# Kernel optimization log

Measured on AMD Instinct MI355X. Metric: run time of the kernel, lower is better.

Reference implementation:

```python
import jax, jax.numpy as jnp
import numpy as np

B, N, H = 8, 256, 768
P = 128          # path_hidden_size
HEADS = 12
D = H // HEADS   # 64
EPS = 1e-5


def layer_norm(x, g, b):
    mu = jnp.mean(x, axis=-1, keepdims=True)
    var = jnp.mean((x - mu) ** 2, axis=-1, keepdims=True)
    return (x - mu) * jax.lax.rsqrt(var + EPS) * g + b


def setup_inputs() -> dict:
    key = jax.random.key(0)
    ks = jax.random.split(key, 16)
    s = 0.02
    return {
        "nodes": jax.random.normal(ks[0], (B, N, H), jnp.float32),
        "bias": jax.random.normal(ks[1], (B, HEADS, N, N), jnp.float32),
        "paths": jax.random.normal(ks[2], (B, N, N, P), jnp.float32),
        "Wq": jax.random.normal(ks[3], (H, H), jnp.float32) * s,
        "bq": jnp.zeros((H,), jnp.float32),
        "Wk": jax.random.normal(ks[4], (H, H), jnp.float32) * s,
        "bk": jnp.zeros((H,), jnp.float32),
        "Wv": jax.random.normal(ks[5], (H, H), jnp.float32) * s,
        "bv": jnp.zeros((H,), jnp.float32),
        "Wsk": jax.random.normal(ks[6], (P, D), jnp.float32) * s,
        "bsk": jnp.zeros((D,), jnp.float32),
        "Wsv": jax.random.normal(ks[7], (P, D), jnp.float32) * s,
        "bsv": jnp.zeros((D,), jnp.float32),
        "Wo": jax.random.normal(ks[8], (H, H), jnp.float32) * s,
        "bo": jnp.zeros((H,), jnp.float32),
        "g_path": jnp.ones((P,), jnp.float32),
        "b_path": jnp.zeros((P,), jnp.float32),
        "g_out": jnp.ones((H,), jnp.float32),
        "b_out": jnp.zeros((H,), jnp.float32),
    }


def reference(nodes, bias, paths, Wq, bq, Wk, bk, Wv, bv, Wsk, bsk, Wsv, bsv,
              Wo, bo, g_path, b_path, g_out, b_out):
    # q/k/v: [B,N,H] -> [B,heads,N,D]
    def split(x):
        return x.reshape(B, N, HEADS, D).transpose(0, 2, 1, 3)

    q = split(nodes @ Wq + bq)
    k = split(nodes @ Wk + bk)
    v = split(nodes @ Wv + bv)

    pn = layer_norm(paths, g_path, b_path)          # [B,N,N,P]
    struct_k = pn @ Wsk + bsk                       # [B,N,N,D]
    struct_v = pn @ Wsv + bsv                       # [B,N,N,D]

    q = q * (D ** -0.5)
    # content scores + per-query-row structural scores + bias
    w = (jnp.einsum('bhqd,bhkd->bhqk', q, k)
         + jnp.einsum('bhqd,bqkd->bhqk', q, struct_k)
         + bias)
    w = jax.nn.softmax(w, axis=-1)                  # [B,heads,N,N]

    out = (jnp.einsum('bhqk,bhkd->bhqd', w, v)
           + jnp.einsum('bhqk,bqkd->bhqd', w, struct_v))
    out = out.transpose(0, 2, 1, 3).reshape(B, N, H)  # combine heads
    out = jax.nn.relu(out @ Wo + bo)
    # dropout is identity in eval mode
    return layer_norm(nodes + out, g_out, b_out)
```

## Files before the change

kernel.cpp:

```cpp
#include <hip/hip_runtime.h>
#include <stdint.h>

#define Bb 8
#define Nn 256
#define Hh 768
#define Pp 128
#define HEADS 12
#define Dd 64
#define EPSf 1e-5f

typedef __attribute__((ext_vector_type(8))) short bhalf8;
typedef __attribute__((ext_vector_type(4))) float f32x4;

__device__ __forceinline__ unsigned short f2bf(float f) {
    union { float f; unsigned u; } v; v.f = f;
    unsigned r = v.u + 0x7FFFu + ((v.u >> 16) & 1u);
    return (unsigned short)(r >> 16);
}
__device__ __forceinline__ float bflo(unsigned u) {
    union { unsigned u; float f; } v; v.u = u << 16; return v.f;
}
__device__ __forceinline__ float bfhi(unsigned u) {
    union { unsigned u; float f; } v; v.u = u & 0xFFFF0000u; return v.f;
}

__global__ __launch_bounds__(256) void k_transpose_bf16(const float* __restrict__ in,
                                                        unsigned short* __restrict__ out,
                                                        int R, int C) {
    __shared__ float tile[32][33];
    int c0 = blockIdx.x * 32, r0 = blockIdx.y * 32;
    int tx = threadIdx.x & 31, ty = threadIdx.x >> 5;
    for (int i = ty; i < 32; i += 8) {
        int r = r0 + i, c = c0 + tx;
        tile[i][tx] = (r < R && c < C) ? in[(size_t)r * C + c] : 0.f;
    }
    __syncthreads();
    for (int i = ty; i < 32; i += 8) {
        int c = c0 + i, r = r0 + tx;
        if (c < C && r < R) out[(size_t)c * R + r] = f2bf(tile[tx][i]);
    }
}

__global__ __launch_bounds__(256) void k_qkv(const float* __restrict__ nodes,
                                             const unsigned short* __restrict__ Wt,
                                             const float* __restrict__ bq, const float* __restrict__ bk,
                                             const float* __restrict__ bv,
                                             float* __restrict__ qs, float* __restrict__ kk,
                                             float* __restrict__ vv) {
    __shared__ __align__(16) unsigned short Alds[64 * 72];
    __shared__ __align__(16) unsigned short Blds[128 * 72];
    int tid = threadIdx.x;
    int m0 = blockIdx.y * 64;
    int n0 = blockIdx.x * 128;
    int w = tid >> 6, lane = tid & 63;
    int wm = w >> 1, wn = w & 1;
    int lm = lane & 15, lq = lane >> 4;
    f32x4 acc[2][4];
#pragma unroll
    for (int i = 0; i < 2; i++)
#pragma unroll
        for (int j = 0; j < 4; j++) acc[i][j] = (f32x4){0.f, 0.f, 0.f, 0.f};

    for (int kt = 0; kt < 768; kt += 64) {
#pragma unroll
        for (int t = 0; t < 4; t++) {
            int c = t * 256 + tid;
            int row = c >> 4, cc = c & 15;
            float4 v = *(const float4*)(nodes + (size_t)(m0 + row) * 768 + kt + cc * 4);
            unsigned u0 = (unsigned)f2bf(v.x) | ((unsigned)f2bf(v.y) << 16);
            unsigned u1 = (unsigned)f2bf(v.z) | ((unsigned)f2bf(v.w) << 16);
            uint2 uu; uu.x = u0; uu.y = u1;
            *(uint2*)(Alds + row * 72 + cc * 4) = uu;
        }
#pragma unroll
        for (int t = 0; t < 4; t++) {
            int c = t * 256 + tid;
            int n = c >> 3, kc = c & 7;
            uint4 v = *(const uint4*)(Wt + (size_t)(n0 + n) * 768 + kt + kc * 8);
            *(uint4*)(Blds + n * 72 + kc * 8) = v;
        }
        __syncthreads();
#pragma unroll
        for (int ks = 0; ks < 2; ks++) {
            bhalf8 af[2];
#pragma unroll
            for (int mi = 0; mi < 2; mi++)
                af[mi] = *(const bhalf8*)(Alds + (wm * 32 + mi * 16 + lm) * 72 + ks * 32 + lq * 8);
#pragma unroll
            for (int nt = 0; nt < 4; nt++) {
                bhalf8 bf = *(const bhalf8*)(Blds + (wn * 64 + nt * 16 + lm) * 72 + ks * 32 + lq * 8);
#pragma unroll
                for (int mi = 0; mi < 2; mi++)
                    acc[mi][nt] = __builtin_amdgcn_mfma_f32_16x16x32_bf16(af[mi], bf, acc[mi][nt], 0, 0, 0);
            }
        }
        __syncthreads();
    }
    int wsel = n0 / 768;
    int nb = n0 % 768;
    const float* bias = (wsel == 0) ? bq : (wsel == 1) ? bk : bv;
    float* dst = (wsel == 0) ? qs : (wsel == 1) ? kk : vv;
    float scale = (wsel == 0) ? 0.125f : 1.0f;
#pragma unroll
    for (int mi = 0; mi < 2; mi++)
#pragma unroll
        for (int nt = 0; nt < 4; nt++)
#pragma unroll
            for (int r = 0; r < 4; r++) {
                int row = m0 + wm * 32 + mi * 16 + lq * 4 + r;
                int col = nb + wn * 64 + nt * 16 + lm;
                int hh = col >> 6, d = col & 63;
                int b = row >> 8, qn = row & 255;
                float val = (acc[mi][nt][r] + bias[col]) * scale;
                dst[(((size_t)b * HEADS + hh) * Nn + qn) * Dd + d] = val;
            }
}

__global__ __launch_bounds__(256) void k_scores(const float* __restrict__ qs,
                                                const float* __restrict__ kk,
                                                const float* __restrict__ bias,
                                                float* __restrict__ wg) {
    __shared__ __align__(16) unsigned short Alds[64 * 72];
    __shared__ __align__(16) unsigned short Blds[64 * 72];
    int tid = threadIdx.x;
    int bh = blockIdx.z;
    int m0 = blockIdx.y * 64;
    int n0 = blockIdx.x * 64;
    int w = tid >> 6, lane = tid & 63, lm = lane & 15, lq = lane >> 4;
    const float* Abase = qs + ((size_t)bh * Nn + m0) * Dd;
    const float* Bbase = kk + ((size_t)bh * Nn + n0) * Dd;
#pragma unroll
    for (int t = 0; t < 4; t++) {
        int c = t * 256 + tid;
        int row = c >> 4, cc = c & 15;
        float4 va = *(const float4*)(Abase + (size_t)row * 64 + cc * 4);
        uint2 ua;
        ua.x = (unsigned)f2bf(va.x) | ((unsigned)f2bf(va.y) << 16);
        ua.y = (unsigned)f2bf(va.z) | ((unsigned)f2bf(va.w) << 16);
        *(uint2*)(Alds + row * 72 + cc * 4) = ua;
        float4 vb = *(const float4*)(Bbase + (size_t)row * 64 + cc * 4);
        uint2 ub;
        ub.x = (unsigned)f2bf(vb.x) | ((unsigned)f2bf(vb.y) << 16);
        ub.y = (unsigned)f2bf(vb.z) | ((unsigned)f2bf(vb.w) << 16);
        *(uint2*)(Blds + row * 72 + cc * 4) = ub;
    }
    __syncthreads();
    f32x4 acc[4];
#pragma unroll
    for (int i = 0; i < 4; i++) acc[i] = (f32x4){0.f, 0.f, 0.f, 0.f};
#pragma unroll
    for (int ks = 0; ks < 2; ks++) {
        bhalf8 af = *(const bhalf8*)(Alds + (w * 16 + lm) * 72 + ks * 32 + lq * 8);
#pragma unroll
        for (int nt = 0; nt < 4; nt++) {
            bhalf8 bf = *(const bhalf8*)(Blds + (nt * 16 + lm) * 72 + ks * 32 + lq * 8);
            acc[nt] = __builtin_amdgcn_mfma_f32_16x16x32_bf16(af, bf, acc[nt], 0, 0, 0);
        }
    }
#pragma unroll
    for (int nt = 0; nt < 4; nt++)
#pragma unroll
        for (int r = 0; r < 4; r++) {
            int row = m0 + w * 16 + lq * 4 + r;
            int col = n0 + nt * 16 + lm;
            size_t idx = ((size_t)bh * Nn + row) * Nn + col;
            wg[idx] = acc[nt][r] + bias[idx];
        }
}

__global__ __launch_bounds__(256) void k_structproj(const float* __restrict__ paths,
                                                    const unsigned short* __restrict__ Wskvt,
                                                    const float* __restrict__ gp, const float* __restrict__ bp,
                                                    const float* __restrict__ bsk, const float* __restrict__ bsv,
                                                    unsigned short* __restrict__ skv) {
    __shared__ __align__(16) unsigned short pn[64 * 136];
    __shared__ __align__(16) unsigned short Bt[128 * 136];
    int tid = threadIdx.x;
    size_t r0 = (size_t)blockIdx.x * 64;
    int w = tid >> 6, lane = tid & 63, lm = lane & 15, lq = lane >> 4;
#pragma unroll
    for (int t = 0; t < 8; t++) {
        int c = t * 256 + tid;
        int n = c >> 4, kc = c & 15;
        uint4 v = *(const uint4*)(Wskvt + n * 128 + kc * 8);
        *(uint4*)(Bt + n * 136 + kc * 8) = v;
    }
    float2 g2 = *(const float2*)(gp + lane * 2);
    float2 b2 = *(const float2*)(bp + lane * 2);
    float2 xr[16];
#pragma unroll
    for (int i = 0; i < 16; i++) {
        size_t row = r0 + w * 16 + i;
        xr[i] = *(const float2*)(paths + row * 128 + lane * 2);
    }
#pragma unroll
    for (int i = 0; i < 16; i++) {
        float2 x = xr[i];
        float s = x.x + x.y, s2 = x.x * x.x + x.y * x.y;
#pragma unroll
        for (int mk = 32; mk; mk >>= 1) {
            s += __shfl_xor(s, mk);
            s2 += __shfl_xor(s2, mk);
        }
        float mu = s * (1.f / 128.f);
        float var = s2 * (1.f / 128.f) - mu * mu;
        float rs = rsqrtf(var + EPSf);
        float p0 = (x.x - mu) * rs * g2.x + b2.x;
        float p1 = (x.y - mu) * rs * g2.y + b2.y;
        unsigned u = (unsigned)f2bf(p0) | ((unsigned)f2bf(p1) << 16);
        *(unsigned*)(pn + (w * 16 + i) * 136 + lane * 2) = u;
    }
    __syncthreads();
    f32x4 acc[8];
#pragma unroll
    for (int i = 0; i < 8; i++) acc[i] = (f32x4){0.f, 0.f, 0.f, 0.f};
#pragma unroll
    for (int ks = 0; ks < 4; ks++) {
        bhalf8 af = *(const bhalf8*)(pn + (w * 16 + lm) * 136 + ks * 32 + lq * 8);
#pragma unroll
        for (int nt = 0; nt < 8; nt++) {
            bhalf8 bf = *(const bhalf8*)(Bt + (nt * 16 + lm) * 136 + ks * 32 + lq * 8);
            acc[nt] = __builtin_amdgcn_mfma_f32_16x16x32_bf16(af, bf, acc[nt], 0, 0, 0);
        }
    }
#pragma unroll
    for (int nt = 0; nt < 8; nt++) {
        int col = nt * 16 + lm;
        float bias = (col < 64) ? bsk[col] : bsv[col - 64];
#pragma unroll
        for (int r = 0; r < 4; r++) {
            size_t grow = r0 + w * 16 + lq * 4 + r;
            skv[grow * 128 + col] = f2bf(acc[nt][r] + bias);
        }
    }
}

__global__ __launch_bounds__(256) void k_attn(const float* __restrict__ qs,
                                              const unsigned short* __restrict__ skv,
                                              float* __restrict__ wg,
                                              float* __restrict__ attn) {
    __shared__ __align__(16) unsigned skl[256 * 36];
    __shared__ __align__(16) float qv[12 * 64];
    __shared__ __align__(16) float wl[12 * 260];
    __shared__ float redm[4], reds[4];
    int tid = threadIdx.x;
    int bq = blockIdx.x;
    int b = bq >> 8, q = bq & 255;
    int lane = tid & 63, wid = tid >> 6;
#pragma unroll
    for (int i = 0; i < 3; i++) {
        int idx = i * 256 + tid;
        int h = idx >> 6, d = idx & 63;
        qv[idx] = qs[(((size_t)b * HEADS + h) * Nn + q) * Dd + d];
    }
    const unsigned short* rowb = skv + (size_t)bq * 256 * 128;
#pragma unroll
    for (int i = 0; i < 8; i++) {
        int c = i * 256 + tid;
        int k = c >> 3, j = c & 7;
        uint4 v = *(const uint4*)(rowb + (size_t)k * 128 + j * 8);
        *(uint4*)(skl + k * 36 + j * 4) = v;
    }
    __syncthreads();
    for (int h = 0; h < 12; h++) {
        float s = 0.f;
#pragma unroll
        for (int j = 0; j < 32; j++) {
            unsigned u = skl[tid * 36 + j];
            float2 q2 = *(const float2*)(qv + h * 64 + 2 * j);
            s += q2.x * bflo(u) + q2.y * bfhi(u);
        }
        size_t widx = (((size_t)b * HEADS + h) * Nn + q) * Nn;
        s += wg[widx + tid];
        float m = s;
#pragma unroll
        for (int mk = 32; mk; mk >>= 1) m = fmaxf(m, __shfl_xor(m, mk));
        if (lane == 0) redm[wid] = m;
        __syncthreads();
        m = fmaxf(fmaxf(redm[0], redm[1]), fmaxf(redm[2], redm[3]));
        float p = __expf(s - m);
        float ps = p;
#pragma unroll
        for (int mk = 32; mk; mk >>= 1) ps += __shfl_xor(ps, mk);
        if (lane == 0) reds[wid] = ps;
        __syncthreads();
        float sum = reds[0] + reds[1] + reds[2] + reds[3];
        float pr = p / sum;
        wl[h * 260 + tid] = pr;
        wg[widx + tid] = pr;
        __syncthreads();
    }
#pragma unroll
    for (int i = 0; i < 8; i++) {
        int c = i * 256 + tid;
        int k = c >> 3, j = c & 7;
        uint4 v = *(const uint4*)(rowb + (size_t)k * 128 + 64 + j * 8);
        *(uint4*)(skl + k * 36 + j * 4) = v;
    }
    __syncthreads();
#pragma unroll
    for (int i = 0; i < 3; i++) {
        int idx = i * 256 + tid;
        int h = idx >> 6, d = idx & 63;
        int jw = d >> 1;
        float o = 0.f;
        if (d & 1) {
            for (int k = 0; k < 256; k += 4) {
                float4 w4 = *(const float4*)(wl + h * 260 + k);
                o += w4.x * bfhi(skl[(k + 0) * 36 + jw]);
                o += w4.y * bfhi(skl[(k + 1) * 36 + jw]);
                o += w4.z * bfhi(skl[(k + 2) * 36 + jw]);
                o += w4.w * bfhi(skl[(k + 3) * 36 + jw]);
            }
        } else {
            for (int k = 0; k < 256; k += 4) {
                float4 w4 = *(const float4*)(wl + h * 260 + k);
                o += w4.x * bflo(skl[(k + 0) * 36 + jw]);
                o += w4.y * bflo(skl[(k + 1) * 36 + jw]);
                o += w4.z * bflo(skl[(k + 2) * 36 + jw]);
                o += w4.w * bflo(skl[(k + 3) * 36 + jw]);
            }
        }
        attn[(size_t)bq * Hh + idx] = o;
    }
}

__global__ __launch_bounds__(256) void k_ctxout(const float* __restrict__ wg,
                                                const float* __restrict__ vv,
                                                float* __restrict__ attn) {
    __shared__ __align__(16) float Al[64 * 68];
    __shared__ __align__(16) float Bl[64 * 68];
    int tid = threadIdx.x;
    int bh = blockIdx.y;
    int m0 = blockIdx.x * 64;
    int b = bh / 12, h = bh % 12;
    int tx = tid & 15, ty = tid >> 4;
    int c0 = tx * 4, r0 = ty * 4;
    float acc[4][4];
#pragma unroll
    for (int i = 0; i < 4; i++)
#pragma unroll
        for (int j = 0; j < 4; j++) acc[i][j] = 0.f;
    const float* Abase = wg + ((size_t)bh * Nn + m0) * Nn;
    const float* Bbase = vv + (size_t)bh * Nn * Dd;
    for (int kt = 0; kt < 256; kt += 64) {
#pragma unroll
        for (int t = 0; t < 4; t++) {
            int c = t * 256 + tid;
            int row = c >> 4, cc = c & 15;
            *(float4*)(Al + row * 68 + cc * 4) = *(const float4*)(Abase + (size_t)row * 256 + kt + cc * 4);
            *(float4*)(Bl + row * 68 + cc * 4) = *(const float4*)(Bbase + (size_t)(kt + row) * 64 + cc * 4);
        }
        __syncthreads();
#pragma unroll 8
        for (int k = 0; k < 64; k++) {
            float4 bv4 = *(const float4*)(Bl + k * 68 + c0);
            float a0 = Al[(r0 + 0) * 68 + k];
            float a1 = Al[(r0 + 1) * 68 + k];
            float a2 = Al[(r0 + 2) * 68 + k];
            float a3 = Al[(r0 + 3) * 68 + k];
            acc[0][0] += a0 * bv4.x; acc[0][1] += a0 * bv4.y; acc[0][2] += a0 * bv4.z; acc[0][3] += a0 * bv4.w;
            acc[1][0] += a1 * bv4.x; acc[1][1] += a1 * bv4.y; acc[1][2] += a1 * bv4.z; acc[1][3] += a1 * bv4.w;
            acc[2][0] += a2 * bv4.x; acc[2][1] += a2 * bv4.y; acc[2][2] += a2 * bv4.z; acc[2][3] += a2 * bv4.w;
            acc[3][0] += a3 * bv4.x; acc[3][1] += a3 * bv4.y; acc[3][2] += a3 * bv4.z; acc[3][3] += a3 * bv4.w;
        }
        __syncthreads();
    }
#pragma unroll
    for (int i = 0; i < 4; i++)
#pragma unroll
        for (int j = 0; j < 4; j++) {
            size_t o = ((size_t)b * Nn + m0 + r0 + i) * Hh + h * 64 + c0 + j;
            attn[o] += acc[i][j];
        }
}

__global__ __launch_bounds__(256) void k_outproj(const float* __restrict__ attn,
                                                 const unsigned short* __restrict__ Wot,
                                                 const float* __restrict__ bo,
                                                 const float* __restrict__ nodes,
                                                 float* __restrict__ tmp) {
    __shared__ __align__(16) unsigned short Alds[64 * 72];
    __shared__ __align__(16) unsigned short Blds[128 * 72];
    int tid = threadIdx.x;
    int m0 = blockIdx.y * 64;
    int n0 = blockIdx.x * 128;
    int w = tid >> 6, lane = tid & 63;
    int wm = w >> 1, wn = w & 1;
    int lm = lane & 15, lq = lane >> 4;
    f32x4 acc[2][4];
#pragma unroll
    for (int i = 0; i < 2; i++)
#pragma unroll
        for (int j = 0; j < 4; j++) acc[i][j] = (f32x4){0.f, 0.f, 0.f, 0.f};
    for (int kt = 0; kt < 768; kt += 64) {
#pragma unroll
        for (int t = 0; t < 4; t++) {
            int c = t * 256 + tid;
            int row = c >> 4, cc = c & 15;
            float4 v = *(const float4*)(attn + (size_t)(m0 + row) * 768 + kt + cc * 4);
            uint2 uu;
            uu.x = (unsigned)f2bf(v.x) | ((unsigned)f2bf(v.y) << 16);
            uu.y = (unsigned)f2bf(v.z) | ((unsigned)f2bf(v.w) << 16);
            *(uint2*)(Alds + row * 72 + cc * 4) = uu;
        }
#pragma unroll
        for (int t = 0; t < 4; t++) {
            int c = t * 256 + tid;
            int n = c >> 3, kc = c & 7;
            uint4 v = *(const uint4*)(Wot + (size_t)(n0 + n) * 768 + kt + kc * 8);
            *(uint4*)(Blds + n * 72 + kc * 8) = v;
        }
        __syncthreads();
#pragma unroll
        for (int ks = 0; ks < 2; ks++) {
            bhalf8 af[2];
#pragma unroll
            for (int mi = 0; mi < 2; mi++)
                af[mi] = *(const bhalf8*)(Alds + (wm * 32 + mi * 16 + lm) * 72 + ks * 32 + lq * 8);
#pragma unroll
            for (int nt = 0; nt < 4; nt++) {
                bhalf8 bf = *(const bhalf8*)(Blds + (wn * 64 + nt * 16 + lm) * 72 + ks * 32 + lq * 8);
#pragma unroll
                for (int mi = 0; mi < 2; mi++)
                    acc[mi][nt] = __builtin_amdgcn_mfma_f32_16x16x32_bf16(af[mi], bf, acc[mi][nt], 0, 0, 0);
            }
        }
        __syncthreads();
    }
#pragma unroll
    for (int mi = 0; mi < 2; mi++)
#pragma unroll
        for (int nt = 0; nt < 4; nt++)
#pragma unroll
            for (int r = 0; r < 4; r++) {
                int row = m0 + wm * 32 + mi * 16 + lq * 4 + r;
                int col = n0 + wn * 64 + nt * 16 + lm;
                float val = acc[mi][nt][r] + bo[col];
                val = fmaxf(val, 0.f) + nodes[(size_t)row * 768 + col];
                tmp[(size_t)row * 768 + col] = val;
            }
}

__global__ __launch_bounds__(256) void k_finalln(const float* __restrict__ tmp,
                                                 const float* __restrict__ go,
                                                 const float* __restrict__ bout,
                                                 float* __restrict__ out) {
    __shared__ float rs1[4], rs2[4];
    int m = blockIdx.x, tid = threadIdx.x;
    int lane = tid & 63, wid = tid >> 6;
    const float* row = tmp + (size_t)m * 768;
    float x0 = row[tid], x1 = row[tid + 256], x2 = row[tid + 512];
    float s = x0 + x1 + x2;
    float s2 = x0 * x0 + x1 * x1 + x2 * x2;
#pragma unroll
    for (int mk = 32; mk; mk >>= 1) {
        s += __shfl_xor(s, mk);
        s2 += __shfl_xor(s2, mk);
    }
    if (lane == 0) { rs1[wid] = s; rs2[wid] = s2; }
    __syncthreads();
    s = rs1[0] + rs1[1] + rs1[2] + rs1[3];
    s2 = rs2[0] + rs2[1] + rs2[2] + rs2[3];
    float mu = s * (1.f / 768.f);
    float var = s2 * (1.f / 768.f) - mu * mu;
    float rstd = rsqrtf(var + EPSf);
    float* orow = out + (size_t)m * 768;
    orow[tid] = (x0 - mu) * rstd * go[tid] + bout[tid];
    orow[tid + 256] = (x1 - mu) * rstd * go[tid + 256] + bout[tid + 256];
    orow[tid + 512] = (x2 - mu) * rstd * go[tid + 512] + bout[tid + 512];
}

extern "C" void kernel_launch(void* const* d_in, const int* in_sizes, int n_in,
                              void* d_out, int out_size, void* d_ws, size_t ws_size,
                              hipStream_t stream) {
    const float* nodes = (const float*)d_in[0];
    const float* bias  = (const float*)d_in[1];
    const float* paths = (const float*)d_in[2];
    const float* Wq = (const float*)d_in[3];  const float* bq  = (const float*)d_in[4];
    const float* Wk = (const float*)d_in[5];  const float* bk  = (const float*)d_in[6];
    const float* Wv = (const float*)d_in[7];  const float* bv  = (const float*)d_in[8];
    const float* Wsk = (const float*)d_in[9]; const float* bsk = (const float*)d_in[10];
    const float* Wsv = (const float*)d_in[11];const float* bsv = (const float*)d_in[12];
    const float* Wo = (const float*)d_in[13]; const float* bo  = (const float*)d_in[14];
    const float* gp = (const float*)d_in[15]; const float* bp  = (const float*)d_in[16];
    const float* go = (const float*)d_in[17]; const float* bout= (const float*)d_in[18];
    float* out = (float*)d_out;

    char* ws = (char*)d_ws;
    size_t off = 0;
    auto carve = [&](size_t bytes) -> char* {
        char* p = ws + off;
        off += (bytes + 255) & ~(size_t)255;
        return p;
    };
    float* qs   = (float*)carve((size_t)Bb * HEADS * Nn * Dd * 4);
    float* kk   = (float*)carve((size_t)Bb * HEADS * Nn * Dd * 4);
    float* vv   = (float*)carve((size_t)Bb * HEADS * Nn * Dd * 4);
    float* wg   = (float*)carve((size_t)Bb * HEADS * Nn * Nn * 4);
    float* attn = (float*)carve((size_t)Bb * Nn * Hh * 4);
    float* tmp  = (float*)carve((size_t)Bb * Nn * Hh * 4);
    unsigned short* Wqkvt = (unsigned short*)carve((size_t)3 * 768 * 768 * 2);
    unsigned short* Wot   = (unsigned short*)carve((size_t)768 * 768 * 2);
    unsigned short* Wskvt = (unsigned short*)carve((size_t)128 * 128 * 2);
    unsigned short* skv   = (unsigned short*)carve((size_t)Bb * Nn * Nn * 128 * 2);
    (void)ws_size; (void)in_sizes; (void)n_in; (void)out_size;

    hipLaunchKernelGGL(k_transpose_bf16, dim3(24, 24), dim3(256), 0, stream, Wq, Wqkvt, 768, 768);
    hipLaunchKernelGGL(k_transpose_bf16, dim3(24, 24), dim3(256), 0, stream, Wk, Wqkvt + (size_t)768 * 768, 768, 768);
    hipLaunchKernelGGL(k_transpose_bf16, dim3(24, 24), dim3(256), 0, stream, Wv, Wqkvt + (size_t)2 * 768 * 768, 768, 768);
    hipLaunchKernelGGL(k_transpose_bf16, dim3(24, 24), dim3(256), 0, stream, Wo, Wot, 768, 768);
    hipLaunchKernelGGL(k_transpose_bf16, dim3(2, 4), dim3(256), 0, stream, Wsk, Wskvt, 128, 64);
    hipLaunchKernelGGL(k_transpose_bf16, dim3(2, 4), dim3(256), 0, stream, Wsv, Wskvt + (size_t)64 * 128, 128, 64);

    hipLaunchKernelGGL(k_qkv, dim3(18, 32), dim3(256), 0, stream, nodes, Wqkvt, bq, bk, bv, qs, kk, vv);
    hipLaunchKernelGGL(k_scores, dim3(4, 4, 96), dim3(256), 0, stream, qs, kk, bias, wg);
    hipLaunchKernelGGL(k_structproj, dim3(8192), dim3(256), 0, stream, paths, Wskvt, gp, bp, bsk, bsv, skv);
    hipLaunchKernelGGL(k_attn, dim3(2048), dim3(256), 0, stream, qs, skv, wg, attn);
    hipLaunchKernelGGL(k_ctxout, dim3(4, 96), dim3(256), 0, stream, wg, vv, attn);
    hipLaunchKernelGGL(k_outproj, dim3(6, 32), dim3(256), 0, stream, attn, Wot, bo, nodes, tmp);
    hipLaunchKernelGGL(k_finalln, dim3(2048), dim3(256), 0, stream, tmp, go, bout, out);
}
```

Baseline: 671.6 us.

## Use MFMA for per-query structural attention and coalesce structproj stores

The per-query attention kernel now computes the structural scores (q·struct_k) and the weighted sum over struct_v with bf16 MFMA instructions. It pads the 12 heads to 16 rows, replacing the scalar FMA loops that ran a barrier-heavy softmax once per head. The structural projection kernel loads paths with float4 and a 16-lane reduction, then stages its output through LDS so the bf16 writes to skv are coalesced 16-byte stores. The weight transposes are merged into two launches. The risks are wasted MFMA rows from the padding, bf16 rounding of q and the softmax probabilities, and strided scalar LDS gathers when building the B operand.

After: 557.4 us. 1.2x faster.

```diff
diff --git a/kernel.cpp b/kernel.cpp
--- a/kernel.cpp
+++ b/kernel.cpp
@@ -17,28 +17,39 @@
     unsigned r = v.u + 0x7FFFu + ((v.u >> 16) & 1u);
     return (unsigned short)(r >> 16);
 }
-__device__ __forceinline__ float bflo(unsigned u) {
-    union { unsigned u; float f; } v; v.u = u << 16; return v.f;
-}
-__device__ __forceinline__ float bfhi(unsigned u) {
-    union { unsigned u; float f; } v; v.u = u & 0xFFFF0000u; return v.f;
-}
-
-__global__ __launch_bounds__(256) void k_transpose_bf16(const float* __restrict__ in,
-                                                        unsigned short* __restrict__ out,
-                                                        int R, int C) {
+
+__global__ __launch_bounds__(256) void k_transpose4(const float* __restrict__ a0, const float* __restrict__ a1,
+                                                    const float* __restrict__ a2, const float* __restrict__ a3,
+                                                    unsigned short* __restrict__ o0, unsigned short* __restrict__ o1,
+                                                    unsigned short* __restrict__ o2, unsigned short* __restrict__ o3) {
     __shared__ float tile[32][33];
+    int z = blockIdx.z;
+    const float* in = (z == 0) ? a0 : (z == 1) ? a1 : (z == 2) ? a2 : a3;
+    unsigned short* out = (z == 0) ? o0 : (z == 1) ? o1 : (z == 2) ? o2 : o3;
+    const int R = 768, C = 768;
     int c0 = blockIdx.x * 32, r0 = blockIdx.y * 32;
     int tx = threadIdx.x & 31, ty = threadIdx.x >> 5;
-    for (int i = ty; i < 32; i += 8) {
-        int r = r0 + i, c = c0 + tx;
-        tile[i][tx] = (r < R && c < C) ? in[(size_t)r * C + c] : 0.f;
-    }
-    __syncthreads();
-    for (int i = ty; i < 32; i += 8) {
-        int c = c0 + i, r = r0 + tx;
-        if (c < C && r < R) out[(size_t)c * R + r] = f2bf(tile[tx][i]);
-    }
+    for (int i = ty; i < 32; i += 8)
+        tile[i][tx] = in[(size_t)(r0 + i) * C + c0 + tx];
+    __syncthreads();
+    for (int i = ty; i < 32; i += 8)
+        out[(size_t)(c0 + i) * R + r0 + tx] = f2bf(tile[tx][i]);
+}
+
+__global__ __launch_bounds__(256) void k_transpose_small(const float* __restrict__ a0, const float* __restrict__ a1,
+                                                         unsigned short* __restrict__ o0, unsigned short* __restrict__ o1) {
+    __shared__ float tile[32][33];
+    int z = blockIdx.z;
+    const float* in = (z == 0) ? a0 : a1;
+    unsigned short* out = (z == 0) ? o0 : o1;
+    const int R = 128, C = 64;
+    int c0 = blockIdx.x * 32, r0 = blockIdx.y * 32;
+    int tx = threadIdx.x & 31, ty = threadIdx.x >> 5;
+    for (int i = ty; i < 32; i += 8)
+        tile[i][tx] = in[(size_t)(r0 + i) * C + c0 + tx];
+    __syncthreads();
+    for (int i = ty; i < 32; i += 8)
+        out[(size_t)(c0 + i) * R + r0 + tx] = f2bf(tile[tx][i]);
 }
 
 __global__ __launch_bounds__(256) void k_qkv(const float* __restrict__ nodes,
@@ -67,9 +78,9 @@
             int c = t * 256 + tid;
             int row = c >> 4, cc = c & 15;
             float4 v = *(const float4*)(nodes + (size_t)(m0 + row) * 768 + kt + cc * 4);
-            unsigned u0 = (unsigned)f2bf(v.x) | ((unsigned)f2bf(v.y) << 16);
-            unsigned u1 = (unsigned)f2bf(v.z) | ((unsigned)f2bf(v.w) << 16);
-            uint2 uu; uu.x = u0; uu.y = u1;
+            uint2 uu;
+            uu.x = (unsigned)f2bf(v.x) | ((unsigned)f2bf(v.y) << 16);
+            uu.y = (unsigned)f2bf(v.z) | ((unsigned)f2bf(v.w) << 16);
             *(uint2*)(Alds + row * 72 + cc * 4) = uu;
         }
 #pragma unroll
@@ -185,30 +196,43 @@
         uint4 v = *(const uint4*)(Wskvt + n * 128 + kc * 8);
         *(uint4*)(Bt + n * 136 + kc * 8) = v;
     }
-    float2 g2 = *(const float2*)(gp + lane * 2);
-    float2 b2 = *(const float2*)(bp + lane * 2);
-    float2 xr[16];
-#pragma unroll
-    for (int i = 0; i < 16; i++) {
-        size_t row = r0 + w * 16 + i;
-        xr[i] = *(const float2*)(paths + row * 128 + lane * 2);
-    }
-#pragma unroll
-    for (int i = 0; i < 16; i++) {
-        float2 x = xr[i];
-        float s = x.x + x.y, s2 = x.x * x.x + x.y * x.y;
-#pragma unroll
-        for (int mk = 32; mk; mk >>= 1) {
+    float4 g0 = *(const float4*)(gp + lm * 4);
+    float4 g1 = *(const float4*)(gp + 64 + lm * 4);
+    float4 bb0 = *(const float4*)(bp + lm * 4);
+    float4 bb1 = *(const float4*)(bp + 64 + lm * 4);
+#pragma unroll
+    for (int it = 0; it < 4; it++) {
+        int row_l = w * 16 + it * 4 + lq;
+        size_t row = r0 + row_l;
+        const float* pr = paths + row * 128;
+        float4 x0 = *(const float4*)(pr + lm * 4);
+        float4 x1 = *(const float4*)(pr + 64 + lm * 4);
+        float s = (x0.x + x0.y) + (x0.z + x0.w) + (x1.x + x1.y) + (x1.z + x1.w);
+        float s2 = x0.x * x0.x + x0.y * x0.y + x0.z * x0.z + x0.w * x0.w
+                 + x1.x * x1.x + x1.y * x1.y + x1.z * x1.z + x1.w * x1.w;
+#pragma unroll
+        for (int mk = 1; mk < 16; mk <<= 1) {
             s += __shfl_xor(s, mk);
             s2 += __shfl_xor(s2, mk);
         }
         float mu = s * (1.f / 128.f);
         float var = s2 * (1.f / 128.f) - mu * mu;
         float rs = rsqrtf(var + EPSf);
-        float p0 = (x.x - mu) * rs * g2.x + b2.x;
-        float p1 = (x.y - mu) * rs * g2.y + b2.y;
-        unsigned u = (unsigned)f2bf(p0) | ((unsigned)f2bf(p1) << 16);
-        *(unsigned*)(pn + (w * 16 + i) * 136 + lane * 2) = u;
+        float p0 = (x0.x - mu) * rs * g0.x + bb0.x;
+        float p1 = (x0.y - mu) * rs * g0.y + bb0.y;
+        float p2 = (x0.z - mu) * rs * g0.z + bb0.z;
+        float p3 = (x0.w - mu) * rs * g0.w + bb0.w;
+        float p4 = (x1.x - mu) * rs * g1.x + bb1.x;
+        float p5 = (x1.y - mu) * rs * g1.y + bb1.y;
+        float p6 = (x1.z - mu) * rs * g1.z + bb1.z;
+        float p7 = (x1.w - mu) * rs * g1.w + bb1.w;
+        uint2 ua, ub;
+        ua.x = (unsigned)f2bf(p0) | ((unsigned)f2bf(p1) << 16);
+        ua.y = (unsigned)f2bf(p2) | ((unsigned)f2bf(p3) << 16);
+        ub.x = (unsigned)f2bf(p4) | ((unsigned)f2bf(p5) << 16);
+        ub.y = (unsigned)f2bf(p6) | ((unsigned)f2bf(p7) << 16);
+        *(uint2*)(pn + row_l * 136 + lm * 4) = ua;
+        *(uint2*)(pn + row_l * 136 + 64 + lm * 4) = ub;
     }
     __syncthreads();
     f32x4 acc[8];
@@ -223,15 +247,24 @@
             acc[nt] = __builtin_amdgcn_mfma_f32_16x16x32_bf16(af, bf, acc[nt], 0, 0, 0);
         }
     }
+    __syncthreads();
 #pragma unroll
     for (int nt = 0; nt < 8; nt++) {
         int col = nt * 16 + lm;
         float bias = (col < 64) ? bsk[col] : bsv[col - 64];
 #pragma unroll
         for (int r = 0; r < 4; r++) {
-            size_t grow = r0 + w * 16 + lq * 4 + r;
-            skv[grow * 128 + col] = f2bf(acc[nt][r] + bias);
-        }
+            int row_l = w * 16 + lq * 4 + r;
+            pn[row_l * 136 + col] = f2bf(acc[nt][r] + bias);
+        }
+    }
+    __syncthreads();
+#pragma unroll
+    for (int i = 0; i < 4; i++) {
+        int c = i * 256 + tid;
+        int row = c >> 4, chunk = c & 15;
+        uint4 v = *(const uint4*)(pn + row * 136 + chunk * 8);
+        *(uint4*)(skv + (r0 + row) * 128 + chunk * 8) = v;
     }
 }
 
@@ -239,19 +272,27 @@
                                               const unsigned short* __restrict__ skv,
                                               float* __restrict__ wg,
                                               float* __restrict__ attn) {
-    __shared__ __align__(16) unsigned skl[256 * 36];
-    __shared__ __align__(16) float qv[12 * 64];
-    __shared__ __align__(16) float wl[12 * 260];
-    __shared__ float redm[4], reds[4];
+    __shared__ __align__(16) unsigned short SKV[256 * 72];
+    __shared__ __align__(16) unsigned short A2[16 * 264];
+    __shared__ __align__(16) unsigned short Ql[16 * 72];
+    __shared__ float redm[16][4];
+    __shared__ float reds[16][4];
     int tid = threadIdx.x;
     int bq = blockIdx.x;
     int b = bq >> 8, q = bq & 255;
-    int lane = tid & 63, wid = tid >> 6;
-#pragma unroll
-    for (int i = 0; i < 3; i++) {
-        int idx = i * 256 + tid;
-        int h = idx >> 6, d = idx & 63;
-        qv[idx] = qs[(((size_t)b * HEADS + h) * Nn + q) * Dd + d];
+    int w = tid >> 6, lane = tid & 63, lm = lane & 15, lq = lane >> 4;
+    if (tid < 192) {
+        int h = tid >> 4, dc = (tid & 15) * 4;
+        float4 v = *(const float4*)(qs + (((size_t)b * HEADS + h) * Nn + q) * Dd + dc);
+        uint2 u;
+        u.x = (unsigned)f2bf(v.x) | ((unsigned)f2bf(v.y) << 16);
+        u.y = (unsigned)f2bf(v.z) | ((unsigned)f2bf(v.w) << 16);
+        *(uint2*)(Ql + h * 72 + dc) = u;
+    } else {
+        int t = tid - 192;
+        int h = 12 + (t >> 4), dc = (t & 15) * 4;
+        uint2 z; z.x = 0; z.y = 0;
+        *(uint2*)(Ql + h * 72 + dc) = z;
     }
     const unsigned short* rowb = skv + (size_t)bq * 256 * 128;
 #pragma unroll
@@ -259,69 +300,106 @@
         int c = i * 256 + tid;
         int k = c >> 3, j = c & 7;
         uint4 v = *(const uint4*)(rowb + (size_t)k * 128 + j * 8);
-        *(uint4*)(skl + k * 36 + j * 4) = v;
-    }
-    __syncthreads();
-    for (int h = 0; h < 12; h++) {
-        float s = 0.f;
-#pragma unroll
-        for (int j = 0; j < 32; j++) {
-            unsigned u = skl[tid * 36 + j];
-            float2 q2 = *(const float2*)(qv + h * 64 + 2 * j);
-            s += q2.x * bflo(u) + q2.y * bfhi(u);
-        }
-        size_t widx = (((size_t)b * HEADS + h) * Nn + q) * Nn;
-        s += wg[widx + tid];
-        float m = s;
-#pragma unroll
-        for (int mk = 32; mk; mk >>= 1) m = fmaxf(m, __shfl_xor(m, mk));
-        if (lane == 0) redm[wid] = m;
-        __syncthreads();
-        m = fmaxf(fmaxf(redm[0], redm[1]), fmaxf(redm[2], redm[3]));
-        float p = __expf(s - m);
-        float ps = p;
-#pragma unroll
-        for (int mk = 32; mk; mk >>= 1) ps += __shfl_xor(ps, mk);
-        if (lane == 0) reds[wid] = ps;
-        __syncthreads();
-        float sum = reds[0] + reds[1] + reds[2] + reds[3];
-        float pr = p / sum;
-        wl[h * 260 + tid] = pr;
-        wg[widx + tid] = pr;
-        __syncthreads();
-    }
+        *(uint4*)(SKV + k * 72 + j * 8) = v;
+    }
+    __syncthreads();
+    f32x4 acc1[4];
+#pragma unroll
+    for (int i = 0; i < 4; i++) acc1[i] = (f32x4){0.f, 0.f, 0.f, 0.f};
+#pragma unroll
+    for (int ks = 0; ks < 2; ks++) {
+        bhalf8 af = *(const bhalf8*)(Ql + lm * 72 + ks * 32 + lq * 8);
+#pragma unroll
+        for (int nt = 0; nt < 4; nt++) {
+            int n0 = (w * 4 + nt) * 16;
+            bhalf8 bf = *(const bhalf8*)(SKV + (n0 + lm) * 72 + ks * 32 + lq * 8);
+            acc1[nt] = __builtin_amdgcn_mfma_f32_16x16x32_bf16(af, bf, acc1[nt], 0, 0, 0);
+        }
+    }
+    size_t wbase = ((size_t)b * HEADS) * Nn * Nn + (size_t)q * Nn;
+    float S[4][4];
+#pragma unroll
+    for (int nt = 0; nt < 4; nt++)
+#pragma unroll
+        for (int r = 0; r < 4; r++) {
+            int row = lq * 4 + r;
+            int col = (w * 4 + nt) * 16 + lm;
+            float wgv = (row < 12) ? wg[wbase + (size_t)row * (Nn * Nn) + col] : 0.f;
+            S[nt][r] = acc1[nt][r] + wgv;
+        }
+    float m4[4];
+#pragma unroll
+    for (int r = 0; r < 4; r++)
+        m4[r] = fmaxf(fmaxf(S[0][r], S[1][r]), fmaxf(S[2][r], S[3][r]));
+#pragma unroll
+    for (int mk = 1; mk < 16; mk <<= 1)
+#pragma unroll
+        for (int r = 0; r < 4; r++) m4[r] = fmaxf(m4[r], __shfl_xor(m4[r], mk));
+    if (lm == 0) {
+#pragma unroll
+        for (int r = 0; r < 4; r++) redm[lq * 4 + r][w] = m4[r];
+    }
+    __syncthreads();
+    float rowmax[4];
+#pragma unroll
+    for (int r = 0; r < 4; r++) {
+        int row = lq * 4 + r;
+        rowmax[r] = fmaxf(fmaxf(redm[row][0], redm[row][1]), fmaxf(redm[row][2], redm[row][3]));
+    }
+    float P[4][4], psum[4];
+#pragma unroll
+    for (int r = 0; r < 4; r++) {
+#pragma unroll
+        for (int nt = 0; nt < 4; nt++) P[nt][r] = __expf(S[nt][r] - rowmax[r]);
+        psum[r] = (P[0][r] + P[1][r]) + (P[2][r] + P[3][r]);
+    }
+#pragma unroll
+    for (int mk = 1; mk < 16; mk <<= 1)
+#pragma unroll
+        for (int r = 0; r < 4; r++) psum[r] += __shfl_xor(psum[r], mk);
+    if (lm == 0) {
+#pragma unroll
+        for (int r = 0; r < 4; r++) reds[lq * 4 + r][w] = psum[r];
+    }
+    __syncthreads();
+    float inv[4];
+#pragma unroll
+    for (int r = 0; r < 4; r++) {
+        int row = lq * 4 + r;
+        inv[r] = 1.f / (((reds[row][0] + reds[row][1]) + (reds[row][2] + reds[row][3])));
+    }
+#pragma unroll
+    for (int nt = 0; nt < 4; nt++)
+#pragma unroll
+        for (int r = 0; r < 4; r++) {
+            int row = lq * 4 + r;
+            int col = (w * 4 + nt) * 16 + lm;
+            float p = P[nt][r] * inv[r];
+            A2[row * 264 + col] = f2bf(p);
+            if (row < 12) wg[wbase + (size_t)row * (Nn * Nn) + col] = p;
+        }
 #pragma unroll
     for (int i = 0; i < 8; i++) {
         int c = i * 256 + tid;
         int k = c >> 3, j = c & 7;
         uint4 v = *(const uint4*)(rowb + (size_t)k * 128 + 64 + j * 8);
-        *(uint4*)(skl + k * 36 + j * 4) = v;
-    }
-    __syncthreads();
-#pragma unroll
-    for (int i = 0; i < 3; i++) {
-        int idx = i * 256 + tid;
-        int h = idx >> 6, d = idx & 63;
-        int jw = d >> 1;
-        float o = 0.f;
-        if (d & 1) {
-            for (int k = 0; k < 256; k += 4) {
-                float4 w4 = *(const float4*)(wl + h * 260 + k);
-                o += w4.x * bfhi(skl[(k + 0) * 36 + jw]);
-                o += w4.y * bfhi(skl[(k + 1) * 36 + jw]);
-                o += w4.z * bfhi(skl[(k + 2) * 36 + jw]);
-                o += w4.w * bfhi(skl[(k + 3) * 36 + jw]);
-            }
-        } else {
-            for (int k = 0; k < 256; k += 4) {
-                float4 w4 = *(const float4*)(wl + h * 260 + k);
-                o += w4.x * bflo(skl[(k + 0) * 36 + jw]);
-                o += w4.y * bflo(skl[(k + 1) * 36 + jw]);
-                o += w4.z * bflo(skl[(k + 2) * 36 + jw]);
-                o += w4.w * bflo(skl[(k + 3) * 36 + jw]);
-            }
-        }
-        attn[(size_t)bq * Hh + idx] = o;
+        *(uint4*)(SKV + k * 72 + j * 8) = v;
+    }
+    __syncthreads();
+    f32x4 acc2 = (f32x4){0.f, 0.f, 0.f, 0.f};
+#pragma unroll
+    for (int ks = 0; ks < 8; ks++) {
+        bhalf8 af = *(const bhalf8*)(A2 + lm * 264 + ks * 32 + lq * 8);
+        bhalf8 bf;
+#pragma unroll
+        for (int j = 0; j < 8; j++)
+            bf[j] = (short)SKV[(ks * 32 + lq * 8 + j) * 72 + w * 16 + lm];
+        acc2 = __builtin_amdgcn_mfma_f32_16x16x32_bf16(af, bf, acc2, 0, 0, 0);
+    }
+#pragma unroll
+    for (int r = 0; r < 4; r++) {
+        int row = lq * 4 + r;
+        if (row < 12) attn[(size_t)bq * Hh + row * 64 + w * 16 + lm] = acc2[r];
     }
 }
 
@@ -506,12 +584,11 @@
     unsigned short* skv   = (unsigned short*)carve((size_t)Bb * Nn * Nn * 128 * 2);
     (void)ws_size; (void)in_sizes; (void)n_in; (void)out_size;
 
-    hipLaunchKernelGGL(k_transpose_bf16, dim3(24, 24), dim3(256), 0, stream, Wq, Wqkvt, 768, 768);
-    hipLaunchKernelGGL(k_transpose_bf16, dim3(24, 24), dim3(256), 0, stream, Wk, Wqkvt + (size_t)768 * 768, 768, 768);
-    hipLaunchKernelGGL(k_transpose_bf16, dim3(24, 24), dim3(256), 0, stream, Wv, Wqkvt + (size_t)2 * 768 * 768, 768, 768);
-    hipLaunchKernelGGL(k_transpose_bf16, dim3(24, 24), dim3(256), 0, stream, Wo, Wot, 768, 768);
-    hipLaunchKernelGGL(k_transpose_bf16, dim3(2, 4), dim3(256), 0, stream, Wsk, Wskvt, 128, 64);
-    hipLaunchKernelGGL(k_transpose_bf16, dim3(2, 4), dim3(256), 0, stream, Wsv, Wskvt + (size_t)64 * 128, 128, 64);
+    hipLaunchKernelGGL(k_transpose4, dim3(24, 24, 4), dim3(256), 0, stream,
+                       Wq, Wk, Wv, Wo,
+                       Wqkvt, Wqkvt + (size_t)768 * 768, Wqkvt + (size_t)2 * 768 * 768, Wot);
+    hipLaunchKernelGGL(k_transpose_small, dim3(2, 4, 2), dim3(256), 0, stream,
+                       Wsk, Wsv, Wskvt, Wskvt + (size_t)64 * 128);
 
     hipLaunchKernelGGL(k_qkv, dim3(18, 32), dim3(256), 0, stream, nodes, Wqkvt, bq, bk, bv, qs, kk, vv);
     hipLaunchKernelGGL(k_scores, dim3(4, 4, 96), dim3(256), 0, stream, qs, kk, bias, wg);
```
